# Kernel tuning notes

Measured on AMD Instinct MI355X. Metric: run time of the kernel, lower is better.

Reference implementation:

```python
import jax, jax.numpy as jnp
import numpy as np

N_NODES = 50000
N_EDGES = 400000
H = 64          # node hidden state dim (entities_dimensions['node'])
E_DIM = 8       # edge_params dim (message.extra_parameters)
MSG_HID = 128   # message-creation MLP hidden width
RD_HID = 128    # readout hidden width
T = 2           # message-passing steps


def setup_inputs() -> dict:
    key = jax.random.key(0)
    ks = jax.random.split(key, 12)
    def w(k, shape):
        return jax.random.normal(k, shape, dtype=jnp.float32) * 0.05
    return {
        "node_feats": jax.random.normal(ks[0], (N_NODES, H), dtype=jnp.float32),
        "edge_feats": jax.random.normal(ks[1], (N_EDGES, E_DIM), dtype=jnp.float32),
        "edge_src": jax.random.randint(ks[2], (N_EDGES,), 0, N_NODES),
        "edge_dst": jax.random.randint(ks[3], (N_EDGES,), 0, N_NODES),
        # message creation MLP: concat(hs_src, hs_dst, edge_params) -> relu -> H
        "W_msg1": w(ks[4], (2 * H + E_DIM, MSG_HID)),
        "b_msg1": jnp.zeros((MSG_HID,), jnp.float32),
        "W_msg2": w(ks[5], (MSG_HID, H)),
        "b_msg2": jnp.zeros((H,), jnp.float32),
        # GRU cell update (keras GRUCell convention, reset_after=False)
        "W_x": w(ks[6], (H, 3 * H)),
        "W_h": w(ks[7], (H, 3 * H)),
        "b_gru": jnp.zeros((3 * H,), jnp.float32),
        # readout MLP: H -> relu -> 1
        "W_r1": w(ks[8], (H, RD_HID)),
        "b_r1": jnp.zeros((RD_HID,), jnp.float32),
        "W_r2": w(ks[9], (RD_HID, 1)),
        "b_r2": jnp.zeros((1,), jnp.float32),
    }


def _gru_cell(h, x, W_x, W_h, b):
    # gates order: update (z), reset (r), candidate (h~) — keras convention
    gx = x @ W_x + b
    gh = h @ W_h
    xz, xr, xh = jnp.split(gx, 3, axis=-1)
    hz, hr, hh = jnp.split(gh, 3, axis=-1)
    z = jax.nn.sigmoid(xz + hz)
    r = jax.nn.sigmoid(xr + hr)
    hc = jnp.tanh(xh + r * hh)
    return z * h + (1.0 - z) * hc


def reference(node_feats, edge_feats, edge_src, edge_dst,
              W_msg1, b_msg1, W_msg2, b_msg2,
              W_x, W_h, b_gru, W_r1, b_r1, W_r2, b_r2):
    h = node_feats  # [N, H] hidden states initialized from entity features
    for _ in range(T):
        # gather source/destination node states per edge: [E, H]
        src_h = h[edge_src]
        dst_h = h[edge_dst]
        m_in = jnp.concatenate([src_h, dst_h, edge_feats], axis=-1)  # [E, 2H+E_DIM]
        m = jax.nn.relu(m_in @ W_msg1 + b_msg1) @ W_msg2 + b_msg2    # [E, H]
        # scatter-sum aggregation to destination nodes: [N, H]
        agg = jax.ops.segment_sum(m, edge_dst, num_segments=N_NODES)
        # recurrent (GRU) node-state update
        h = _gru_cell(h, agg, W_x, W_h, b_gru)
    # readout MLP on final hidden states
    out = jax.nn.relu(h @ W_r1 + b_r1) @ W_r2 + b_r2  # [N, 1]
    return out
```

## Files before the change

### kernel.cpp

```cpp
#include <hip/hip_runtime.h>
#include <hip/hip_bf16.h>

#define NN 50000
#define NE 400000
#define NGRP 25000
#define NCH 196
#define NPAD 50176

typedef __bf16 bf16_t;
typedef __bf16 bf16x4 __attribute__((ext_vector_type(4)));
typedef __bf16 bf16x8 __attribute__((ext_vector_type(8)));
typedef float  floatx4 __attribute__((ext_vector_type(4)));

static __device__ __forceinline__ floatx4 mfma16(bf16x8 a, bf16x8 b, floatx4 c) {
    return __builtin_amdgcn_mfma_f32_16x16x32_bf16(a, b, c, 0, 0, 0);
}
static __device__ __forceinline__ float sigm_f(float x) {
    return 1.f / (1.f + __expf(-x));
}
static __device__ __forceinline__ float tanh_f(float x) {
    return 1.f - 2.f / (__expf(2.f * x) + 1.f);
}
static __device__ __forceinline__ bf16x8 cvt8(const float* sp) {
    float4 f0 = *(const float4*)sp;
    float4 f1 = *(const float4*)(sp + 4);
    bf16x8 v;
    v[0] = (bf16_t)f0.x; v[1] = (bf16_t)f0.y; v[2] = (bf16_t)f0.z; v[3] = (bf16_t)f0.w;
    v[4] = (bf16_t)f1.x; v[5] = (bf16_t)f1.y; v[6] = (bf16_t)f1.z; v[7] = (bf16_t)f1.w;
    return v;
}

__global__ __launch_bounds__(256) void prep_kernel(
    const float* __restrict__ nf,
    const float* __restrict__ Wm1, const float* __restrict__ Wm2,
    const float* __restrict__ Wx,  const float* __restrict__ Wh,
    const float* __restrict__ Wr1,
    bf16_t* __restrict__ hb,
    bf16_t* __restrict__ W1f, bf16_t* __restrict__ W2f,
    bf16_t* __restrict__ Wxt, bf16_t* __restrict__ Wht,
    bf16_t* __restrict__ Wr1f)
{
    int u = blockIdx.x * 256 + threadIdx.x;
    if (u < 800000) {
        float4 v = *(const float4*)(nf + (size_t)u * 4);
        bf16x4 o;
        o[0] = (bf16_t)v.x; o[1] = (bf16_t)v.y; o[2] = (bf16_t)v.z; o[3] = (bf16_t)v.w;
        *(bf16x4*)(hb + (size_t)u * 4) = o;
        return;
    }
    u -= 800000;
    if (u < 20480) {
        int j = u & 7, l = (u >> 3) & 63, rem = u >> 9;
        int ks = rem % 5, nt = rem / 5;
        int n = nt * 16 + (l & 15);
        int k = ks * 32 + (l >> 4) * 8 + j;
        W1f[u] = (k < 136) ? (bf16_t)Wm1[k * 128 + n] : (bf16_t)0.f;
        return;
    }
    u -= 20480;
    if (u < 8192) {
        int j = u & 7, l = (u >> 3) & 63, rem = u >> 9;
        int kg = rem & 3, nt = rem >> 2;
        int n = nt * 16 + (l & 15);
        int k = kg * 32 + (l >> 4) * 8 + j;
        W2f[u] = (bf16_t)Wm2[k * 64 + n];
        return;
    }
    u -= 8192;
    if (u < 12288) {
        int n = u >> 6, k = u & 63;
        Wxt[u] = (bf16_t)Wx[k * 192 + n];
        return;
    }
    u -= 12288;
    if (u < 12288) {
        int n = u >> 6, k = u & 63;
        Wht[u] = (bf16_t)Wh[k * 192 + n];
        return;
    }
    u -= 12288;
    if (u < 8192) {
        int j = u & 7, l = (u >> 3) & 63, rem = u >> 9;
        int kg = rem & 1, nt = rem >> 1;
        int n = nt * 16 + (l & 15);
        int k = kg * 32 + (l >> 4) * 8 + j;
        Wr1f[u] = (bf16_t)Wr1[k * 128 + n];
    }
}

__global__ __launch_bounds__(256) void hist_kernel(
    const int* __restrict__ edst, int* __restrict__ deg)
{
    int e = blockIdx.x * 256 + threadIdx.x;
    if (e < NE) atomicAdd(&deg[edst[e]], 1);
}

__global__ __launch_bounds__(256) void scanA_kernel(
    const int* __restrict__ deg, int* __restrict__ chunkSums)
{
    __shared__ int s[256];
    int i = blockIdx.x * 256 + threadIdx.x;
    s[threadIdx.x] = deg[i];
    __syncthreads();
    for (int st = 128; st >= 1; st >>= 1) {
        if (threadIdx.x < st) s[threadIdx.x] += s[threadIdx.x + st];
        __syncthreads();
    }
    if (threadIdx.x == 0) chunkSums[blockIdx.x] = s[0];
}

__global__ __launch_bounds__(256) void scanB_kernel(
    const int* __restrict__ chunkSums, int* __restrict__ chunkOff)
{
    __shared__ int s[256];
    int t = threadIdx.x;
    int v = (t < NCH) ? chunkSums[t] : 0;
    s[t] = v;
    __syncthreads();
    for (int st = 1; st < 256; st <<= 1) {
        int add = (t >= st) ? s[t - st] : 0;
        __syncthreads();
        s[t] += add;
        __syncthreads();
    }
    if (t < NCH) chunkOff[t] = s[t] - v;
}

__global__ __launch_bounds__(256) void scanC_kernel(
    const int* __restrict__ deg, const int* __restrict__ chunkOff,
    int* __restrict__ cursor)
{
    __shared__ int s[256];
    int t = threadIdx.x;
    int i = blockIdx.x * 256 + t;
    int v = deg[i];
    s[t] = v;
    __syncthreads();
    for (int st = 1; st < 256; st <<= 1) {
        int add = (t >= st) ? s[t - st] : 0;
        __syncthreads();
        s[t] += add;
        __syncthreads();
    }
    cursor[i] = chunkOff[blockIdx.x] + s[t] - v;
}

__global__ __launch_bounds__(256) void scatter_kernel(
    const int* __restrict__ esrc, const int* __restrict__ edst,
    const float* __restrict__ ef,
    int* __restrict__ cursor, int* __restrict__ srcs, int* __restrict__ dsts,
    bf16_t* __restrict__ efpb)
{
    int e = blockIdx.x * 256 + threadIdx.x;
    if (e >= NE) return;
    int d = edst[e];
    int p = atomicAdd(&cursor[d], 1);
    srcs[p] = esrc[e];
    dsts[p] = d;
    float4 a = *(const float4*)(ef + (size_t)e * 8);
    float4 b = *(const float4*)(ef + (size_t)e * 8 + 4);
    bf16x8 v;
    v[0] = (bf16_t)a.x; v[1] = (bf16_t)a.y; v[2] = (bf16_t)a.z; v[3] = (bf16_t)a.w;
    v[4] = (bf16_t)b.x; v[5] = (bf16_t)b.y; v[6] = (bf16_t)b.z; v[7] = (bf16_t)b.w;
    *(bf16x8*)(efpb + (size_t)p * 8) = v;
}

__global__ __launch_bounds__(512) void edge_kernel(
    const bf16_t* __restrict__ hb, const bf16_t* __restrict__ efpb,
    const int* __restrict__ srcs, const int* __restrict__ dsts,
    const bf16_t* __restrict__ W1f, const bf16_t* __restrict__ W2f,
    const float* __restrict__ b1f, const float* __restrict__ b2f,
    float* __restrict__ agg)
{
    __shared__ __attribute__((aligned(16))) bf16_t w1s[20480];
    __shared__ __attribute__((aligned(16))) bf16_t w2s[8192];
    __shared__ __attribute__((aligned(16))) bf16_t hq[8][16 * 36];

    const int tid = threadIdx.x;
    {
        const uint4* s1 = (const uint4*)W1f;
        uint4* d1 = (uint4*)w1s;
        #pragma unroll
        for (int i = 0; i < 5; i++) d1[tid + i * 512] = s1[tid + i * 512];
        const uint4* s2 = (const uint4*)W2f;
        uint4* d2 = (uint4*)w2s;
        #pragma unroll
        for (int i = 0; i < 2; i++) d2[tid + i * 512] = s2[tid + i * 512];
    }
    __syncthreads();

    const int lane = tid & 63;
    const int wv   = tid >> 6;
    const int l15  = lane & 15;
    const int quad = lane >> 4;

    float b1r[8], b2r[4];
    #pragma unroll
    for (int nt = 0; nt < 8; nt++) b1r[nt] = b1f[nt * 16 + l15];
    #pragma unroll
    for (int nt = 0; nt < 4; nt++) b2r[nt] = b2f[nt * 16 + l15];

    const int WTOT = gridDim.x * 8;
    int g = blockIdx.x * 8 + wv;

    bf16x8 af[5];
    int4 d4;
    {
        int row = g * 16 + l15;
        int si = srcs[row], di = dsts[row];
        const bf16_t* sp = hb + (size_t)si * 64 + quad * 8;
        const bf16_t* dp = hb + (size_t)di * 64 + quad * 8;
        af[0] = *(const bf16x8*)sp;  af[1] = *(const bf16x8*)(sp + 32);
        af[2] = *(const bf16x8*)dp;  af[3] = *(const bf16x8*)(dp + 32);
        if (quad == 0) {
            af[4] = *(const bf16x8*)(efpb + (size_t)row * 8);
        } else {
            #pragma unroll
            for (int q = 0; q < 8; q++) af[4][q] = (bf16_t)0.f;
        }
        d4 = *(const int4*)(dsts + g * 16 + quad * 4);
    }

    while (true) {
        int gn = g + WTOT;
        int gp = (gn < NGRP) ? gn : g;
        int prow = gp * 16 + l15;
        int si_n = srcs[prow], di_n = dsts[prow];
        int4 d4_n = *(const int4*)(dsts + gp * 16 + quad * 4);

        floatx4 oa[4];
        #pragma unroll
        for (int nt = 0; nt < 4; nt++) { oa[nt].x = 0.f; oa[nt].y = 0.f; oa[nt].z = 0.f; oa[nt].w = 0.f; }

        #pragma unroll
        for (int q = 0; q < 4; q++) {
            floatx4 acc[2];
            #pragma unroll
            for (int nt = 0; nt < 2; nt++) { acc[nt].x = 0.f; acc[nt].y = 0.f; acc[nt].z = 0.f; acc[nt].w = 0.f; }
            #pragma unroll
            for (int nt = 0; nt < 2; nt++) {
                int gnt = q * 2 + nt;
                #pragma unroll
                for (int ks = 0; ks < 5; ks++) {
                    bf16x8 b = *(const bf16x8*)(w1s + ((gnt * 5 + ks) * 64 + lane) * 8);
                    acc[nt] = mfma16(af[ks], b, acc[nt]);
                }
            }
            #pragma unroll
            for (int nt = 0; nt < 2; nt++) {
                float bb = b1r[q * 2 + nt];
                #pragma unroll
                for (int r = 0; r < 4; r++) {
                    float v = fmaxf(acc[nt][r] + bb, 0.f);
                    hq[wv][(quad * 4 + r) * 36 + nt * 16 + l15] = (bf16_t)v;
                }
            }
            bf16x8 hf = *(const bf16x8*)(hq[wv] + l15 * 36 + quad * 8);
            #pragma unroll
            for (int nt = 0; nt < 4; nt++) {
                bf16x8 w2 = *(const bf16x8*)(w2s + ((nt * 4 + q) * 64 + lane) * 8);
                oa[nt] = mfma16(hf, w2, oa[nt]);
            }
        }

        bf16x8 af_n[5];
        {
            const bf16_t* sp = hb + (size_t)si_n * 64 + quad * 8;
            const bf16_t* dp = hb + (size_t)di_n * 64 + quad * 8;
            af_n[0] = *(const bf16x8*)sp;  af_n[1] = *(const bf16x8*)(sp + 32);
            af_n[2] = *(const bf16x8*)dp;  af_n[3] = *(const bf16x8*)(dp + 32);
            if (quad == 0) {
                af_n[4] = *(const bf16x8*)(efpb + (size_t)prow * 8);
            } else {
                #pragma unroll
                for (int q = 0; q < 8; q++) af_n[4][q] = (bf16_t)0.f;
            }
        }

        #pragma unroll
        for (int nt = 0; nt < 4; nt++) {
            int col = nt * 16 + l15;
            float bb = b2r[nt];
            float* ap = agg + col;
            int dcur = d4.x;
            float v = oa[nt][0] + bb;
            if (d4.y == dcur) v += oa[nt][1] + bb;
            else { atomicAdd(ap + (size_t)dcur * 64, v); dcur = d4.y; v = oa[nt][1] + bb; }
            if (d4.z == dcur) v += oa[nt][2] + bb;
            else { atomicAdd(ap + (size_t)dcur * 64, v); dcur = d4.z; v = oa[nt][2] + bb; }
            if (d4.w == dcur) v += oa[nt][3] + bb;
            else { atomicAdd(ap + (size_t)dcur * 64, v); dcur = d4.w; v = oa[nt][3] + bb; }
            atomicAdd(ap + (size_t)dcur * 64, v);
        }

        if (gn >= NGRP) break;
        g = gn;
        #pragma unroll
        for (int i = 0; i < 5; i++) af[i] = af_n[i];
        d4 = d4_n;
    }
}

template<int LAST>
__global__ __launch_bounds__(256) void gru_kernel(
    const float* __restrict__ agg, const float* __restrict__ h_in,
    float* __restrict__ h_out, bf16_t* __restrict__ hb_out,
    const bf16_t* __restrict__ Wxt, const bf16_t* __restrict__ Wht,
    const float* __restrict__ bg,
    const bf16_t* __restrict__ Wr1f, const float* __restrict__ br1,
    const float* __restrict__ Wr2, const float* __restrict__ br2,
    float* __restrict__ out)
{
    __shared__ __attribute__((aligned(16))) float  shd[64 * 68];
    __shared__ __attribute__((aligned(16))) bf16_t hb2[4][16 * 72];
    const int tid = threadIdx.x;
    const int n0  = blockIdx.x * 64;

    for (int idx = tid; idx < 64 * 16; idx += 256) {
        int i = idx >> 4, c = (idx & 15) * 4;
        int n = n0 + i; if (n >= NN) n = NN - 1;
        *(float4*)&shd[i * 68 + c] = *(const float4*)(h_in + (size_t)n * 64 + c);
    }
    __syncthreads();

    const int lane = tid & 63;
    const int wv   = tid >> 6;
    const int l15  = lane & 15;
    const int quad = lane >> 4;
    const int rowA = wv * 16 + l15;
    int nA = n0 + rowA; if (nA >= NN) nA = NN - 1;

    bf16x8 ax[2], ah[2];
    ax[0] = cvt8(agg + (size_t)nA * 64 + quad * 8);
    ax[1] = cvt8(agg + (size_t)nA * 64 + quad * 8 + 32);
    {
        const float* hp = shd + rowA * 68 + quad * 8;
        ah[0] = cvt8(hp);
        ah[1] = cvt8(hp + 32);
    }

    floatx4 az[4], ar[4], axh[4], ahh[4];
    #pragma unroll
    for (int nt = 0; nt < 4; nt++) {
        az[nt].x=0.f; az[nt].y=0.f; az[nt].z=0.f; az[nt].w=0.f;
        ar[nt].x=0.f; ar[nt].y=0.f; ar[nt].z=0.f; ar[nt].w=0.f;
        axh[nt].x=0.f; axh[nt].y=0.f; axh[nt].z=0.f; axh[nt].w=0.f;
        ahh[nt].x=0.f; ahh[nt].y=0.f; ahh[nt].z=0.f; ahh[nt].w=0.f;
    }
    #pragma unroll
    for (int nt = 0; nt < 4; nt++) {
        const bf16_t* bx_z = Wxt + (nt * 16 + l15) * 64 + quad * 8;
        const bf16_t* bh_z = Wht + (nt * 16 + l15) * 64 + quad * 8;
        const bf16_t* bx_r = bx_z + 64 * 64;
        const bf16_t* bh_r = bh_z + 64 * 64;
        const bf16_t* bx_h = bx_z + 128 * 64;
        const bf16_t* bh_h = bh_z + 128 * 64;
        az[nt]  = mfma16(ax[0], *(const bf16x8*)bx_z,        az[nt]);
        az[nt]  = mfma16(ax[1], *(const bf16x8*)(bx_z + 32), az[nt]);
        az[nt]  = mfma16(ah[0], *(const bf16x8*)bh_z,        az[nt]);
        az[nt]  = mfma16(ah[1], *(const bf16x8*)(bh_z + 32), az[nt]);
        ar[nt]  = mfma16(ax[0], *(const bf16x8*)bx_r,        ar[nt]);
        ar[nt]  = mfma16(ax[1], *(const bf16x8*)(bx_r + 32), ar[nt]);
        ar[nt]  = mfma16(ah[0], *(const bf16x8*)bh_r,        ar[nt]);
        ar[nt]  = mfma16(ah[1], *(const bf16x8*)(bh_r + 32), ar[nt]);
        axh[nt] = mfma16(ax[0], *(const bf16x8*)bx_h,        axh[nt]);
        axh[nt] = mfma16(ax[1], *(const bf16x8*)(bx_h + 32), axh[nt]);
        ahh[nt] = mfma16(ah[0], *(const bf16x8*)bh_h,        ahh[nt]);
        ahh[nt] = mfma16(ah[1], *(const bf16x8*)(bh_h + 32), ahh[nt]);
    }

    #pragma unroll
    for (int nt = 0; nt < 4; nt++) {
        int j = nt * 16 + l15;
        float bz = bg[j], brr = bg[64 + j], bh = bg[128 + j];
        #pragma unroll
        for (int r = 0; r < 4; r++) {
            int lrow = wv * 16 + quad * 4 + r;
            int n = n0 + lrow;
            float z  = sigm_f(az[nt][r] + bz);
            float rr = sigm_f(ar[nt][r] + brr);
            float hc = tanh_f(axh[nt][r] + bh + rr * ahh[nt][r]);
            float hold = shd[lrow * 68 + j];
            float hnew = z * hold + (1.f - z) * hc;
            if (LAST) {
                hb2[wv][(quad * 4 + r) * 72 + j] = (bf16_t)hnew;
            } else if (n < NN) {
                h_out[(size_t)n * 64 + j]  = hnew;
                hb_out[(size_t)n * 64 + j] = (bf16_t)hnew;
            }
        }
    }

    if (LAST) {
        bf16x8 a0 = *(const bf16x8*)(hb2[wv] + l15 * 72 + quad * 8);
        bf16x8 a1 = *(const bf16x8*)(hb2[wv] + l15 * 72 + quad * 8 + 32);
        floatx4 accR[8];
        #pragma unroll
        for (int nt = 0; nt < 8; nt++) { accR[nt].x=0.f; accR[nt].y=0.f; accR[nt].z=0.f; accR[nt].w=0.f; }
        #pragma unroll
        for (int nt = 0; nt < 8; nt++) {
            bf16x8 b0 = *(const bf16x8*)(Wr1f + ((nt * 2 + 0) * 64 + lane) * 8);
            bf16x8 b1 = *(const bf16x8*)(Wr1f + ((nt * 2 + 1) * 64 + lane) * 8);
            accR[nt] = mfma16(a0, b0, accR[nt]);
            accR[nt] = mfma16(a1, b1, accR[nt]);
        }
        float br1r[8], wr2r[8];
        #pragma unroll
        for (int nt = 0; nt < 8; nt++) {
            br1r[nt] = br1[nt * 16 + l15];
            wr2r[nt] = Wr2[nt * 16 + l15];
        }
        float br2v = br2[0];
        #pragma unroll
        for (int r = 0; r < 4; r++) {
            float p = 0.f;
            #pragma unroll
            for (int nt = 0; nt < 8; nt++)
                p += fmaxf(accR[nt][r] + br1r[nt], 0.f) * wr2r[nt];
            p += __shfl_xor(p, 1, 64);
            p += __shfl_xor(p, 2, 64);
            p += __shfl_xor(p, 4, 64);
            p += __shfl_xor(p, 8, 64);
            if (l15 == 0) {
                int n = n0 + wv * 16 + quad * 4 + r;
                if (n < NN) out[n] = p + br2v;
            }
        }
    }
}

extern "C" void kernel_launch(void* const* d_in, const int* in_sizes, int n_in,
                              void* d_out, int out_size, void* d_ws, size_t ws_size,
                              hipStream_t stream)
{
    const float* nf  = (const float*)d_in[0];
    const float* ef  = (const float*)d_in[1];
    const int* esrc  = (const int*)d_in[2];
    const int* edst  = (const int*)d_in[3];
    const float* Wm1 = (const float*)d_in[4];
    const float* bm1 = (const float*)d_in[5];
    const float* Wm2 = (const float*)d_in[6];
    const float* bm2 = (const float*)d_in[7];
    const float* Wx  = (const float*)d_in[8];
    const float* Wh  = (const float*)d_in[9];
    const float* bg  = (const float*)d_in[10];
    const float* Wr1 = (const float*)d_in[11];
    const float* br1 = (const float*)d_in[12];
    const float* Wr2 = (const float*)d_in[13];
    const float* br2 = (const float*)d_in[14];

    char* ws = (char*)d_ws;
    float*  hbuf   = (float*)(ws);
    float*  agg    = (float*)(ws + 12800000);
    bf16_t* hb     = (bf16_t*)(ws + 25600000);
    bf16_t* W1f    = (bf16_t*)(ws + 32000000);
    bf16_t* W2f    = (bf16_t*)(ws + 32040960);
    bf16_t* Wxt    = (bf16_t*)(ws + 32057344);
    bf16_t* Wht    = (bf16_t*)(ws + 32081920);
    bf16_t* Wr1f   = (bf16_t*)(ws + 32106496);
    int*    srcs   = (int*)(ws + 32122880);
    int*    dsts   = (int*)(ws + 33722880);
    bf16_t* efpb   = (bf16_t*)(ws + 35322880);
    int*    deg    = (int*)(ws + 41722880);
    int*    cursor = (int*)(ws + 41923584);
    int*    chunkS = (int*)(ws + 42124288);
    int*    chunkO = (int*)(ws + 42125312);

    prep_kernel<<<3365, 256, 0, stream>>>(nf, Wm1, Wm2, Wx, Wh, Wr1,
                                          hb, W1f, W2f, Wxt, Wht, Wr1f);

    hipMemsetAsync(deg, 0, NPAD * 4, stream);
    hist_kernel<<<(NE + 255) / 256, 256, 0, stream>>>(edst, deg);
    scanA_kernel<<<NCH, 256, 0, stream>>>(deg, chunkS);
    scanB_kernel<<<1, 256, 0, stream>>>(chunkS, chunkO);
    scanC_kernel<<<NCH, 256, 0, stream>>>(deg, chunkO, cursor);
    scatter_kernel<<<(NE + 255) / 256, 256, 0, stream>>>(esrc, edst, ef, cursor,
                                                         srcs, dsts, efpb);

    for (int t = 0; t < 2; t++) {
        const float* h_in = (t == 0) ? nf : hbuf;
        hipMemsetAsync(agg, 0, (size_t)NN * 64 * 4, stream);
        edge_kernel<<<512, 512, 0, stream>>>(hb, efpb, srcs, dsts,
                                             W1f, W2f, bm1, bm2, agg);
        if (t == 0) {
            gru_kernel<0><<<(NN + 63) / 64, 256, 0, stream>>>(
                agg, h_in, hbuf, hb, Wxt, Wht, bg,
                Wr1f, br1, Wr2, br2, (float*)d_out);
        } else {
            gru_kernel<1><<<(NN + 63) / 64, 256, 0, stream>>>(
                agg, h_in, nullptr, nullptr, Wxt, Wht, bg,
                Wr1f, br1, Wr2, br2, (float*)d_out);
        }
    }
}
```

Measured before the change: 360.0 us.

## Process two edge tiles per wave and fold agg zeroing into GRU

Each wave of the edge kernel now handles 32 edges (two 16-row MFMA tiles) per iteration, so every LDS weight fragment feeds two MFMAs. Block size drops to 256 threads over 1024 blocks. The per-step agg memset is removed: agg sits right after deg so one memset clears both, and the first GRU pass zeroes agg rows after reading them. This cuts weight-fragment LDS reads and memset launches, at the cost of more registers per wave, which may lower occupancy and latency hiding for the gathers.

```diff
diff --git a/kernel.cpp b/kernel.cpp
--- a/kernel.cpp
+++ b/kernel.cpp
@@ -3,7 +3,7 @@
 
 #define NN 50000
 #define NE 400000
-#define NGRP 25000
+#define NPAIR 12500
 #define NCH 196
 #define NPAD 50176
 
@@ -165,7 +165,7 @@
     *(bf16x8*)(efpb + (size_t)p * 8) = v;
 }
 
-__global__ __launch_bounds__(512) void edge_kernel(
+__global__ __launch_bounds__(256) void edge_kernel(
     const bf16_t* __restrict__ hb, const bf16_t* __restrict__ efpb,
     const int* __restrict__ srcs, const int* __restrict__ dsts,
     const bf16_t* __restrict__ W1f, const bf16_t* __restrict__ W2f,
@@ -174,18 +174,18 @@
 {
     __shared__ __attribute__((aligned(16))) bf16_t w1s[20480];
     __shared__ __attribute__((aligned(16))) bf16_t w2s[8192];
-    __shared__ __attribute__((aligned(16))) bf16_t hq[8][16 * 36];
+    __shared__ __attribute__((aligned(16))) bf16_t hq[4][32 * 36];
 
     const int tid = threadIdx.x;
     {
         const uint4* s1 = (const uint4*)W1f;
         uint4* d1 = (uint4*)w1s;
         #pragma unroll
-        for (int i = 0; i < 5; i++) d1[tid + i * 512] = s1[tid + i * 512];
+        for (int i = 0; i < 10; i++) d1[tid + i * 256] = s1[tid + i * 256];
         const uint4* s2 = (const uint4*)W2f;
         uint4* d2 = (uint4*)w2s;
         #pragma unroll
-        for (int i = 0; i < 2; i++) d2[tid + i * 512] = s2[tid + i * 512];
+        for (int i = 0; i < 4; i++) d2[tid + i * 256] = s2[tid + i * 256];
     }
     __syncthreads();
 
@@ -200,50 +200,68 @@
     #pragma unroll
     for (int nt = 0; nt < 4; nt++) b2r[nt] = b2f[nt * 16 + l15];
 
-    const int WTOT = gridDim.x * 8;
-    int g = blockIdx.x * 8 + wv;
-
-    bf16x8 af[5];
-    int4 d4;
+    const int WTOT = gridDim.x * 4;
+    int p = blockIdx.x * 4 + wv;
+
+    bf16x8 af0[5], af1[5];
+    int4 d40, d41;
     {
-        int row = g * 16 + l15;
-        int si = srcs[row], di = dsts[row];
-        const bf16_t* sp = hb + (size_t)si * 64 + quad * 8;
-        const bf16_t* dp = hb + (size_t)di * 64 + quad * 8;
-        af[0] = *(const bf16x8*)sp;  af[1] = *(const bf16x8*)(sp + 32);
-        af[2] = *(const bf16x8*)dp;  af[3] = *(const bf16x8*)(dp + 32);
+        int base = p * 32;
+        int r0 = base + l15, r1 = base + 16 + l15;
+        int si0 = srcs[r0], di0 = dsts[r0];
+        int si1 = srcs[r1], di1 = dsts[r1];
+        const bf16_t* sp0 = hb + (size_t)si0 * 64 + quad * 8;
+        const bf16_t* dp0 = hb + (size_t)di0 * 64 + quad * 8;
+        const bf16_t* sp1 = hb + (size_t)si1 * 64 + quad * 8;
+        const bf16_t* dp1 = hb + (size_t)di1 * 64 + quad * 8;
+        af0[0] = *(const bf16x8*)sp0;  af0[1] = *(const bf16x8*)(sp0 + 32);
+        af0[2] = *(const bf16x8*)dp0;  af0[3] = *(const bf16x8*)(dp0 + 32);
+        af1[0] = *(const bf16x8*)sp1;  af1[1] = *(const bf16x8*)(sp1 + 32);
+        af1[2] = *(const bf16x8*)dp1;  af1[3] = *(const bf16x8*)(dp1 + 32);
         if (quad == 0) {
-            af[4] = *(const bf16x8*)(efpb + (size_t)row * 8);
+            af0[4] = *(const bf16x8*)(efpb + (size_t)r0 * 8);
+            af1[4] = *(const bf16x8*)(efpb + (size_t)r1 * 8);
         } else {
             #pragma unroll
-            for (int q = 0; q < 8; q++) af[4][q] = (bf16_t)0.f;
-        }
-        d4 = *(const int4*)(dsts + g * 16 + quad * 4);
+            for (int q = 0; q < 8; q++) { af0[4][q] = (bf16_t)0.f; af1[4][q] = (bf16_t)0.f; }
+        }
+        d40 = *(const int4*)(dsts + base + quad * 4);
+        d41 = *(const int4*)(dsts + base + 16 + quad * 4);
     }
 
     while (true) {
-        int gn = g + WTOT;
-        int gp = (gn < NGRP) ? gn : g;
-        int prow = gp * 16 + l15;
-        int si_n = srcs[prow], di_n = dsts[prow];
-        int4 d4_n = *(const int4*)(dsts + gp * 16 + quad * 4);
-
-        floatx4 oa[4];
-        #pragma unroll
-        for (int nt = 0; nt < 4; nt++) { oa[nt].x = 0.f; oa[nt].y = 0.f; oa[nt].z = 0.f; oa[nt].w = 0.f; }
+        int pn = p + WTOT;
+        int pp = (pn < NPAIR) ? pn : p;
+        int nbase = pp * 32;
+        int nr0 = nbase + l15, nr1 = nbase + 16 + l15;
+        int si0n = srcs[nr0], di0n = dsts[nr0];
+        int si1n = srcs[nr1], di1n = dsts[nr1];
+        int4 d40n = *(const int4*)(dsts + nbase + quad * 4);
+        int4 d41n = *(const int4*)(dsts + nbase + 16 + quad * 4);
+
+        floatx4 oa0[4], oa1[4];
+        #pragma unroll
+        for (int nt = 0; nt < 4; nt++) {
+            oa0[nt].x=0.f; oa0[nt].y=0.f; oa0[nt].z=0.f; oa0[nt].w=0.f;
+            oa1[nt].x=0.f; oa1[nt].y=0.f; oa1[nt].z=0.f; oa1[nt].w=0.f;
+        }
 
         #pragma unroll
         for (int q = 0; q < 4; q++) {
-            floatx4 acc[2];
+            floatx4 ac0[2], ac1[2];
             #pragma unroll
-            for (int nt = 0; nt < 2; nt++) { acc[nt].x = 0.f; acc[nt].y = 0.f; acc[nt].z = 0.f; acc[nt].w = 0.f; }
+            for (int nt = 0; nt < 2; nt++) {
+                ac0[nt].x=0.f; ac0[nt].y=0.f; ac0[nt].z=0.f; ac0[nt].w=0.f;
+                ac1[nt].x=0.f; ac1[nt].y=0.f; ac1[nt].z=0.f; ac1[nt].w=0.f;
+            }
             #pragma unroll
             for (int nt = 0; nt < 2; nt++) {
                 int gnt = q * 2 + nt;
                 #pragma unroll
                 for (int ks = 0; ks < 5; ks++) {
                     bf16x8 b = *(const bf16x8*)(w1s + ((gnt * 5 + ks) * 64 + lane) * 8);
-                    acc[nt] = mfma16(af[ks], b, acc[nt]);
+                    ac0[nt] = mfma16(af0[ks], b, ac0[nt]);
+                    ac1[nt] = mfma16(af1[ks], b, ac1[nt]);
                 }
             }
             #pragma unroll
@@ -251,29 +269,34 @@
                 float bb = b1r[q * 2 + nt];
                 #pragma unroll
                 for (int r = 0; r < 4; r++) {
-                    float v = fmaxf(acc[nt][r] + bb, 0.f);
-                    hq[wv][(quad * 4 + r) * 36 + nt * 16 + l15] = (bf16_t)v;
+                    float v0 = fmaxf(ac0[nt][r] + bb, 0.f);
+                    float v1 = fmaxf(ac1[nt][r] + bb, 0.f);
+                    hq[wv][(quad * 4 + r) * 36 + nt * 16 + l15]        = (bf16_t)v0;
+                    hq[wv][(16 + quad * 4 + r) * 36 + nt * 16 + l15]   = (bf16_t)v1;
                 }
             }
-            bf16x8 hf = *(const bf16x8*)(hq[wv] + l15 * 36 + quad * 8);
+            bf16x8 hf0 = *(const bf16x8*)(hq[wv] + l15 * 36 + quad * 8);
+            bf16x8 hf1 = *(const bf16x8*)(hq[wv] + (16 + l15) * 36 + quad * 8);
             #pragma unroll
             for (int nt = 0; nt < 4; nt++) {
                 bf16x8 w2 = *(const bf16x8*)(w2s + ((nt * 4 + q) * 64 + lane) * 8);
-                oa[nt] = mfma16(hf, w2, oa[nt]);
-            }
-        }
-
-        bf16x8 af_n[5];
+                oa0[nt] = mfma16(hf0, w2, oa0[nt]);
+                oa1[nt] = mfma16(hf1, w2, oa1[nt]);
+            }
+        }
+
         {
-            const bf16_t* sp = hb + (size_t)si_n * 64 + quad * 8;
-            const bf16_t* dp = hb + (size_t)di_n * 64 + quad * 8;
-            af_n[0] = *(const bf16x8*)sp;  af_n[1] = *(const bf16x8*)(sp + 32);
-            af_n[2] = *(const bf16x8*)dp;  af_n[3] = *(const bf16x8*)(dp + 32);
+            const bf16_t* sp0 = hb + (size_t)si0n * 64 + quad * 8;
+            const bf16_t* dp0 = hb + (size_t)di0n * 64 + quad * 8;
+            const bf16_t* sp1 = hb + (size_t)si1n * 64 + quad * 8;
+            const bf16_t* dp1 = hb + (size_t)di1n * 64 + quad * 8;
+            af0[0] = *(const bf16x8*)sp0;  af0[1] = *(const bf16x8*)(sp0 + 32);
+            af0[2] = *(const bf16x8*)dp0;  af0[3] = *(const bf16x8*)(dp0 + 32);
+            af1[0] = *(const bf16x8*)sp1;  af1[1] = *(const bf16x8*)(sp1 + 32);
+            af1[2] = *(const bf16x8*)dp1;  af1[3] = *(const bf16x8*)(dp1 + 32);
             if (quad == 0) {
-                af_n[4] = *(const bf16x8*)(efpb + (size_t)prow * 8);
-            } else {
-                #pragma unroll
-                for (int q = 0; q < 8; q++) af_n[4][q] = (bf16_t)0.f;
+                af0[4] = *(const bf16x8*)(efpb + (size_t)nr0 * 8);
+                af1[4] = *(const bf16x8*)(efpb + (size_t)nr1 * 8);
             }
         }
 
@@ -282,28 +305,40 @@
             int col = nt * 16 + l15;
             float bb = b2r[nt];
             float* ap = agg + col;
-            int dcur = d4.x;
-            float v = oa[nt][0] + bb;
-            if (d4.y == dcur) v += oa[nt][1] + bb;
-            else { atomicAdd(ap + (size_t)dcur * 64, v); dcur = d4.y; v = oa[nt][1] + bb; }
-            if (d4.z == dcur) v += oa[nt][2] + bb;
-            else { atomicAdd(ap + (size_t)dcur * 64, v); dcur = d4.z; v = oa[nt][2] + bb; }
-            if (d4.w == dcur) v += oa[nt][3] + bb;
-            else { atomicAdd(ap + (size_t)dcur * 64, v); dcur = d4.w; v = oa[nt][3] + bb; }
-            atomicAdd(ap + (size_t)dcur * 64, v);
-        }
-
-        if (gn >= NGRP) break;
-        g = gn;
-        #pragma unroll
-        for (int i = 0; i < 5; i++) af[i] = af_n[i];
-        d4 = d4_n;
+            {
+                int dcur = d40.x;
+                float v = oa0[nt][0] + bb;
+                if (d40.y == dcur) v += oa0[nt][1] + bb;
+                else { atomicAdd(ap + (size_t)dcur * 64, v); dcur = d40.y; v = oa0[nt][1] + bb; }
+                if (d40.z == dcur) v += oa0[nt][2] + bb;
+                else { atomicAdd(ap + (size_t)dcur * 64, v); dcur = d40.z; v = oa0[nt][2] + bb; }
+                if (d40.w == dcur) v += oa0[nt][3] + bb;
+                else { atomicAdd(ap + (size_t)dcur * 64, v); dcur = d40.w; v = oa0[nt][3] + bb; }
+                atomicAdd(ap + (size_t)dcur * 64, v);
+            }
+            {
+                int dcur = d41.x;
+                float v = oa1[nt][0] + bb;
+                if (d41.y == dcur) v += oa1[nt][1] + bb;
+                else { atomicAdd(ap + (size_t)dcur * 64, v); dcur = d41.y; v = oa1[nt][1] + bb; }
+                if (d41.z == dcur) v += oa1[nt][2] + bb;
+                else { atomicAdd(ap + (size_t)dcur * 64, v); dcur = d41.z; v = oa1[nt][2] + bb; }
+                if (d41.w == dcur) v += oa1[nt][3] + bb;
+                else { atomicAdd(ap + (size_t)dcur * 64, v); dcur = d41.w; v = oa1[nt][3] + bb; }
+                atomicAdd(ap + (size_t)dcur * 64, v);
+            }
+        }
+
+        if (pn >= NPAIR) break;
+        p = pn;
+        d40 = d40n;
+        d41 = d41n;
     }
 }
 
 template<int LAST>
 __global__ __launch_bounds__(256) void gru_kernel(
-    const float* __restrict__ agg, const float* __restrict__ h_in,
+    float* __restrict__ agg, const float* __restrict__ h_in,
     float* __restrict__ h_out, bf16_t* __restrict__ hb_out,
     const bf16_t* __restrict__ Wxt, const bf16_t* __restrict__ Wht,
     const float* __restrict__ bg,
@@ -328,7 +363,8 @@
     const int l15  = lane & 15;
     const int quad = lane >> 4;
     const int rowA = wv * 16 + l15;
-    int nA = n0 + rowA; if (nA >= NN) nA = NN - 1;
+    const bool rowOK = (n0 + rowA) < NN;
+    int nA = n0 + rowA; if (!rowOK) nA = NN - 1;
 
     bf16x8 ax[2], ah[2];
     ax[0] = cvt8(agg + (size_t)nA * 64 + quad * 8);
@@ -337,6 +373,13 @@
         const float* hp = shd + rowA * 68 + quad * 8;
         ah[0] = cvt8(hp);
         ah[1] = cvt8(hp + 32);
+    }
+    if (!LAST && rowOK) {
+        float4 z = make_float4(0.f, 0.f, 0.f, 0.f);
+        *(float4*)(agg + (size_t)nA * 64 + quad * 8)      = z;
+        *(float4*)(agg + (size_t)nA * 64 + quad * 8 + 4)  = z;
+        *(float4*)(agg + (size_t)nA * 64 + quad * 8 + 32) = z;
+        *(float4*)(agg + (size_t)nA * 64 + quad * 8 + 36) = z;
     }
 
     floatx4 az[4], ar[4], axh[4], ahh[4];
@@ -451,17 +494,17 @@
 
     char* ws = (char*)d_ws;
     float*  hbuf   = (float*)(ws);
-    float*  agg    = (float*)(ws + 12800000);
-    bf16_t* hb     = (bf16_t*)(ws + 25600000);
-    bf16_t* W1f    = (bf16_t*)(ws + 32000000);
-    bf16_t* W2f    = (bf16_t*)(ws + 32040960);
-    bf16_t* Wxt    = (bf16_t*)(ws + 32057344);
-    bf16_t* Wht    = (bf16_t*)(ws + 32081920);
-    bf16_t* Wr1f   = (bf16_t*)(ws + 32106496);
-    int*    srcs   = (int*)(ws + 32122880);
-    int*    dsts   = (int*)(ws + 33722880);
-    bf16_t* efpb   = (bf16_t*)(ws + 35322880);
-    int*    deg    = (int*)(ws + 41722880);
+    bf16_t* hb     = (bf16_t*)(ws + 12800000);
+    bf16_t* W1f    = (bf16_t*)(ws + 19200000);
+    bf16_t* W2f    = (bf16_t*)(ws + 19240960);
+    bf16_t* Wxt    = (bf16_t*)(ws + 19257344);
+    bf16_t* Wht    = (bf16_t*)(ws + 19281920);
+    bf16_t* Wr1f   = (bf16_t*)(ws + 19306496);
+    int*    srcs   = (int*)(ws + 19322880);
+    int*    dsts   = (int*)(ws + 20922880);
+    bf16_t* efpb   = (bf16_t*)(ws + 22522880);
+    int*    deg    = (int*)(ws + 28922880);
+    float*  agg    = (float*)(ws + 29123584);
     int*    cursor = (int*)(ws + 41923584);
     int*    chunkS = (int*)(ws + 42124288);
     int*    chunkO = (int*)(ws + 42125312);
@@ -469,7 +512,7 @@
     prep_kernel<<<3365, 256, 0, stream>>>(nf, Wm1, Wm2, Wx, Wh, Wr1,
                                           hb, W1f, W2f, Wxt, Wht, Wr1f);
 
-    hipMemsetAsync(deg, 0, NPAD * 4, stream);
+    hipMemsetAsync(deg, 0, (size_t)NPAD * 4 + (size_t)NN * 64 * 4, stream);
     hist_kernel<<<(NE + 255) / 256, 256, 0, stream>>>(edst, deg);
     scanA_kernel<<<NCH, 256, 0, stream>>>(deg, chunkS);
     scanB_kernel<<<1, 256, 0, stream>>>(chunkS, chunkO);
@@ -477,19 +520,13 @@
     scatter_kernel<<<(NE + 255) / 256, 256, 0, stream>>>(esrc, edst, ef, cursor,
                                                          srcs, dsts, efpb);
 
-    for (int t = 0; t < 2; t++) {
-        const float* h_in = (t == 0) ? nf : hbuf;
-        hipMemsetAsync(agg, 0, (size_t)NN * 64 * 4, stream);
-        edge_kernel<<<512, 512, 0, stream>>>(hb, efpb, srcs, dsts,
-                                             W1f, W2f, bm1, bm2, agg);
-        if (t == 0) {
-            gru_kernel<0><<<(NN + 63) / 64, 256, 0, stream>>>(
-                agg, h_in, hbuf, hb, Wxt, Wht, bg,
-                Wr1f, br1, Wr2, br2, (float*)d_out);
-        } else {
-            gru_kernel<1><<<(NN + 63) / 64, 256, 0, stream>>>(
-                agg, h_in, nullptr, nullptr, Wxt, Wht, bg,
-                Wr1f, br1, Wr2, br2, (float*)d_out);
-        }
-    }
-}
+    edge_kernel<<<1024, 256, 0, stream>>>(hb, efpb, srcs, dsts,
+                                          W1f, W2f, bm1, bm2, agg);
+    gru_kernel<0><<<(NN + 63) / 64, 256, 0, stream>>>(
+        agg, nf, hbuf, hb, Wxt, Wht, bg, Wr1f, br1, Wr2, br2, (float*)d_out);
+    edge_kernel<<<1024, 256, 0, stream>>>(hb, efpb, srcs, dsts,
+                                          W1f, W2f, bm1, bm2, agg);
+    gru_kernel<1><<<(NN + 63) / 64, 256, 0, stream>>>(
+        agg, hbuf, nullptr, nullptr, Wxt, Wht, bg, Wr1f, br1, Wr2, br2,
+        (float*)d_out);
+}
```

Result: no change. 356.4 us (-1.0%).
